# Performance work log

Hardware: AMD Instinct MI355X
Metric: run time of the kernel (lower is better)

The kernel has to match this reference:

```python
import jax, jax.numpy as jnp
import numpy as np

N = 50000      # nodes
E = 800000     # edges
F = 128        # input features
H = 128        # hidden dim
G = 1024       # graphs in batch
EPS = 1e-5


def setup_inputs() -> dict:
    key = jax.random.key(0)
    ks = jax.random.split(key, 16)
    s = 0.05
    return {
        "x": jax.random.normal(ks[0], (N, F), dtype=jnp.float32),
        "edge_index": jax.random.randint(ks[1], (2, E), 0, N, dtype=jnp.int64),
        "batch": jnp.sort(jax.random.randint(ks[2], (N,), 0, G, dtype=jnp.int64)),
        "convW0": jax.random.normal(ks[3], (F, H), dtype=jnp.float32) * s,
        "convW": jax.random.normal(ks[4], (2, H, H), dtype=jnp.float32) * s,  # layers 1,2
        "convb": jax.random.normal(ks[5], (3, H), dtype=jnp.float32) * s,
        "bn_gamma": jnp.ones((3, H), dtype=jnp.float32),
        "bn_beta": jnp.zeros((3, H), dtype=jnp.float32),
        "mW1": jax.random.normal(ks[6], (2 * H, 256), dtype=jnp.float32) * s,
        "mb1": jnp.zeros((256,), dtype=jnp.float32),
        "mW2": jax.random.normal(ks[7], (256, 128), dtype=jnp.float32) * s,
        "mb2": jnp.zeros((128,), dtype=jnp.float32),
        "mW3": jax.random.normal(ks[8], (128, 1), dtype=jnp.float32) * s,
        "mb3": jnp.zeros((1,), dtype=jnp.float32),
    }


def _gcn_norm(edge_index):
    # add self-loops, compute sym-normalization coeffs (PyG GCNConv default)
    loop = jnp.arange(N, dtype=edge_index.dtype)
    src = jnp.concatenate([edge_index[0], loop])
    dst = jnp.concatenate([edge_index[1], loop])
    deg = jax.ops.segment_sum(jnp.ones_like(dst, dtype=jnp.float32), dst, num_segments=N)
    dinv = jax.lax.rsqrt(deg)  # deg >= 1 due to self loops
    norm = dinv[src] * dinv[dst]  # [E+N]
    return src, dst, norm


def _gcn_layer(x, W, b, src, dst, norm):
    h = x @ W                               # [N, H]
    msg = h[src] * norm[:, None]            # gather + scale, [E+N, H]
    agg = jax.ops.segment_sum(msg, dst, num_segments=N)
    return agg + b


def _batchnorm(x, gamma, beta):
    mu = jnp.mean(x, axis=0)
    var = jnp.mean(jnp.square(x - mu), axis=0)  # biased, as torch training fwd
    return gamma * (x - mu) * jax.lax.rsqrt(var + EPS) + beta


def reference(x, edge_index, batch, convW0, convW, convb, bn_gamma, bn_beta,
              mW1, mb1, mW2, mb2, mW3, mb3):
    src, dst, norm = _gcn_norm(edge_index)
    Ws = [convW0, convW[0], convW[1]]
    for i in range(3):
        x = _gcn_layer(x, Ws[i], convb[i], src, dst, norm)
        x = _batchnorm(x, bn_gamma[i], bn_beta[i])
        x = jax.nn.relu(x)
        # dropout: identity in eval mode
    ones = jnp.ones((N,), dtype=x.dtype)
    counts = jax.ops.segment_sum(ones, batch, num_segments=G)  # [G]
    x_mean = jax.ops.segment_sum(x, batch, num_segments=G) / jnp.maximum(counts, 1.0)[:, None]
    x_max = jax.ops.segment_max(x, batch, num_segments=G)
    x_max = jnp.where(counts[:, None] > 0, x_max, 0.0)
    g = jnp.concatenate([x_mean, x_max], axis=1)  # [G, 2H]
    h = jax.nn.relu(g @ mW1 + mb1)
    h = jax.nn.relu(h @ mW2 + mb2)
    out = h @ mW3 + mb3                            # [G, 1]
    return out.squeeze(1)
```

## Files before the change

### kernel.cpp

```cpp
#include <hip/hip_runtime.h>


constexpr int FH = 128;
constexpr int GG = 1024;
constexpr int NAB = 2048;
constexpr int BKS = 1024;
constexpr int CPAD = 16;
constexpr int EPB = 4096;
constexpr float EPSV = 1e-5f;

typedef __attribute__((ext_vector_type(8))) short short8v;
typedef __attribute__((ext_vector_type(4))) float f32x4;

__device__ inline unsigned short bf16_rn(float x) {
    unsigned u = __float_as_uint(x);
    unsigned r = (u + 0x7FFFu + ((u >> 16) & 1u)) >> 16;
    return (unsigned short)r;
}
__device__ inline float bflo(unsigned u) { return __uint_as_float(u << 16); }
__device__ inline float bfhi(unsigned u) { return __uint_as_float(u & 0xFFFF0000u); }
__device__ inline float bfs(unsigned short h) { return __uint_as_float((unsigned)h << 16); }
__device__ inline float4 bf4tof(ushort4 h) {
    return make_float4(bfs(h.x), bfs(h.y), bfs(h.z), bfs(h.w));
}

__global__ void k_deg(const int* __restrict__ dst, unsigned* __restrict__ deg, int E) {
    int e = blockIdx.x * 256 + threadIdx.x;
    if (e < E) atomicAdd(&deg[dst[e]], 1u);
}

__global__ __launch_bounds__(1024) void k_scan1(const unsigned* __restrict__ deg,
                                                int* __restrict__ rowptr, int* __restrict__ bsum,
                                                float* __restrict__ dinv, int n) {
    __shared__ int wsum[16];
    int i = blockIdx.x * 1024 + threadIdx.x;
    int lane = threadIdx.x & 63, wid = threadIdx.x >> 6;
    int v = (i < n) ? (int)deg[i] : 0;
    if (i < n) dinv[i] = rsqrtf((float)v + 1.0f);
    int incl = v;
    #pragma unroll
    for (int off = 1; off < 64; off <<= 1) {
        int t = __shfl_up(incl, off, 64);
        if (lane >= off) incl += t;
    }
    if (lane == 63) wsum[wid] = incl;
    __syncthreads();
    int woff = 0;
    #pragma unroll
    for (int w = 0; w < 16; ++w) woff += (w < wid) ? wsum[w] : 0;
    if (i < n) rowptr[i] = woff + incl - v;
    if (threadIdx.x == 1023) bsum[blockIdx.x] = woff + incl;
}

__global__ void k_scan2(int* __restrict__ bsum, int* __restrict__ rowptr_n, int nb) {
    int lane = threadIdx.x;
    int v = (lane < nb) ? bsum[lane] : 0;
    int incl = v;
    #pragma unroll
    for (int off = 1; off < 64; off <<= 1) {
        int t = __shfl_up(incl, off, 64);
        if (lane >= off) incl += t;
    }
    if (lane < nb) bsum[lane] = incl - v;
    if (lane == 63) *rowptr_n = incl;
}

__global__ __launch_bounds__(1024) void k_scan3(int* __restrict__ rowptr,
                                                const int* __restrict__ bsum,
                                                int* __restrict__ bcur, int n) {
    int i = blockIdx.x * 1024 + threadIdx.x;
    if (i < n) {
        int r = rowptr[i] + bsum[blockIdx.x];
        rowptr[i] = r;
        if ((i & 63) == 0) bcur[(i >> 6) * CPAD] = r;
    }
}

__global__ __launch_bounds__(256) void k_binscatter(const int* __restrict__ src, const int* __restrict__ dst,
                                                    int* __restrict__ bcur, unsigned* __restrict__ tmp,
                                                    int E, int nbk) {
    __shared__ int hist[BKS];
    int tid = threadIdx.x;
    for (int b = tid; b < nbk; b += 256) hist[b] = 0;
    __syncthreads();
    int e0 = blockIdx.x * EPB;
    int s[16], d[16];
    #pragma unroll
    for (int i = 0; i < 16; ++i) {
        int e = e0 + i * 256 + tid;
        if (e < E) {
            s[i] = src[e]; d[i] = dst[e];
            atomicAdd(&hist[d[i] >> 6], 1);
        } else d[i] = -1;
    }
    __syncthreads();
    for (int b = tid; b < nbk; b += 256) {
        int c = hist[b];
        hist[b] = c ? atomicAdd(&bcur[b * CPAD], c) : 0;
    }
    __syncthreads();
    #pragma unroll
    for (int i = 0; i < 16; ++i) {
        if (d[i] >= 0) {
            int p = atomicAdd(&hist[d[i] >> 6], 1);
            tmp[p] = (unsigned)s[i] | ((unsigned)(d[i] & 63) << 16);
        }
    }
}

__global__ __launch_bounds__(256) void k_finesort(const unsigned* __restrict__ tmp,
                                                  const int* __restrict__ rowptr,
                                                  int* __restrict__ csr_src, int n) {
    __shared__ int cur[64];
    int nb0 = blockIdx.x << 6;
    int tid = threadIdx.x;
    int hi = min(nb0 + 64, n);
    if (tid < 64 && nb0 + tid < n) cur[tid] = rowptr[nb0 + tid];
    __syncthreads();
    int estart = rowptr[nb0], eend = rowptr[hi];
    for (int e = estart + tid; e < eend; e += 256) {
        unsigned pr = tmp[e];
        int p = atomicAdd(&cur[(pr >> 16) & 63], 1);
        csr_src[p] = (int)(pr & 0xFFFFu);
    }
}

__global__ void k_gptr(const int* __restrict__ batch, int* __restrict__ gptr, int n) {
    int g = blockIdx.x * 256 + threadIdx.x;
    if (g > GG) return;
    int lo = 0, hi = n;
    while (lo < hi) { int mid = (lo + hi) >> 1; if (batch[mid] < g) lo = mid + 1; else hi = mid; }
    gptr[g] = lo;
}

__global__ void k_wprep(const float* __restrict__ W0, const float* __restrict__ W12,
                        unsigned short* __restrict__ Wt) {
    int t = blockIdx.x * 256 + threadIdx.x;
    int l = t >> 14, o = t & 16383;
    const float* W = (l == 0) ? W0 : W12 + (size_t)(l - 1) * 16384;
    int j = o & 7, c = (o >> 3) & 15, hi = (o >> 7) & 3, kb = (o >> 9) & 3, nt = o >> 11;
    int k = kb * 32 + hi * 8 + j;
    int col = nt * 16 + c;
    Wt[t] = bf16_rn(W[k * 128 + col]);
}

template<bool BF16IN>
__global__ __launch_bounds__(256) void k_gemm(const void* __restrict__ Xp,
                                              const unsigned short* __restrict__ Wt,
                                              const float* __restrict__ dinv,
                                              const float* __restrict__ sc,
                                              const float* __restrict__ sh,
                                              unsigned short* __restrict__ H, int n) {
    int wave = threadIdx.x >> 6, L = threadIdx.x & 63;
    int hi = L >> 4, c16 = L & 15;
    int m0 = blockIdx.x * 64 + wave * 16;
    int arow = m0 + c16;
    bool okA = arow < n;

    short8v aF[4];
    #pragma unroll
    for (int kb = 0; kb < 4; ++kb) {
        int kc = kb * 32 + hi * 8;
        float v[8];
        #pragma unroll
        for (int j = 0; j < 8; ++j) v[j] = 0.f;
        if (okA) {
            if constexpr (BF16IN) {
                const unsigned short* Xb = (const unsigned short*)Xp;
                uint4 raw = *(const uint4*)&Xb[(size_t)arow * 128 + kc];
                v[0] = bflo(raw.x); v[1] = bfhi(raw.x);
                v[2] = bflo(raw.y); v[3] = bfhi(raw.y);
                v[4] = bflo(raw.z); v[5] = bfhi(raw.z);
                v[6] = bflo(raw.w); v[7] = bfhi(raw.w);
                float4 s0 = *(const float4*)&sc[kc], s1 = *(const float4*)&sc[kc + 4];
                float4 h0 = *(const float4*)&sh[kc], h1 = *(const float4*)&sh[kc + 4];
                v[0] = fmaxf(fmaf(v[0], s0.x, h0.x), 0.f);
                v[1] = fmaxf(fmaf(v[1], s0.y, h0.y), 0.f);
                v[2] = fmaxf(fmaf(v[2], s0.z, h0.z), 0.f);
                v[3] = fmaxf(fmaf(v[3], s0.w, h0.w), 0.f);
                v[4] = fmaxf(fmaf(v[4], s1.x, h1.x), 0.f);
                v[5] = fmaxf(fmaf(v[5], s1.y, h1.y), 0.f);
                v[6] = fmaxf(fmaf(v[6], s1.z, h1.z), 0.f);
                v[7] = fmaxf(fmaf(v[7], s1.w, h1.w), 0.f);
            } else {
                const float* Xf = (const float*)Xp;
                float4 v0 = *(const float4*)&Xf[(size_t)arow * 128 + kc];
                float4 v1 = *(const float4*)&Xf[(size_t)arow * 128 + kc + 4];
                v[0] = v0.x; v[1] = v0.y; v[2] = v0.z; v[3] = v0.w;
                v[4] = v1.x; v[5] = v1.y; v[6] = v1.z; v[7] = v1.w;
            }
        }
        short8v a;
        #pragma unroll
        for (int j = 0; j < 8; ++j) a[j] = (short)bf16_rn(v[j]);
        aF[kb] = a;
    }

    f32x4 acc[8];
    #pragma unroll
    for (int nt = 0; nt < 8; ++nt) {
        acc[nt][0] = 0.f; acc[nt][1] = 0.f; acc[nt][2] = 0.f; acc[nt][3] = 0.f;
    }
    #pragma unroll
    for (int nt = 0; nt < 8; ++nt) {
        #pragma unroll
        for (int kb = 0; kb < 4; ++kb) {
            short8v bF = *(const short8v*)&Wt[(size_t)(nt * 4 + kb) * 512 + L * 8];
            acc[nt] = __builtin_amdgcn_mfma_f32_16x16x32_bf16(aF[kb], bF, acc[nt], 0, 0, 0);
        }
    }

    #pragma unroll
    for (int reg = 0; reg < 4; ++reg) {
        int row = m0 + hi * 4 + reg;
        if (row < n) {
            float dv = dinv[row];
            #pragma unroll
            for (int nt = 0; nt < 8; ++nt)
                H[(size_t)row * 128 + nt * 16 + c16] = bf16_rn(acc[nt][reg] * dv);
        }
    }
}

__global__ __launch_bounds__(256) void k_aggstats(const int* __restrict__ rowptr, const int* __restrict__ csr_src,
                                                  const float* __restrict__ dinv,
                                                  const unsigned short* __restrict__ H2,
                                                  unsigned short* __restrict__ Bo,
                                                  float* __restrict__ partials, int n) {
    __shared__ float sb[8][128];
    int tid = threadIdx.x;
    int sub = tid >> 5, lane = tid & 31;
    const ushort4* Hv = (const ushort4*)H2;
    float sA[4] = {0.f, 0.f, 0.f, 0.f}, qA[4] = {0.f, 0.f, 0.f, 0.f};
    for (int node = blockIdx.x * 8 + sub; node < n; node += NAB * 8) {
        int beg = rowptr[node], end = rowptr[node + 1];
        float dv = dinv[node];
        float4 acc = bf4tof(Hv[(size_t)node * 32 + lane]);
        float4 acc2 = make_float4(0.f, 0.f, 0.f, 0.f);
        int e = beg;
        for (; e + 1 < end; e += 2) {
            int s0 = csr_src[e], s1 = csr_src[e + 1];
            float4 h0 = bf4tof(Hv[(size_t)s0 * 32 + lane]);
            float4 h1 = bf4tof(Hv[(size_t)s1 * 32 + lane]);
            acc.x += h0.x;  acc.y += h0.y;  acc.z += h0.z;  acc.w += h0.w;
            acc2.x += h1.x; acc2.y += h1.y; acc2.z += h1.z; acc2.w += h1.w;
        }
        if (e < end) {
            int s0 = csr_src[e];
            float4 h0 = bf4tof(Hv[(size_t)s0 * 32 + lane]);
            acc.x += h0.x; acc.y += h0.y; acc.z += h0.z; acc.w += h0.w;
        }
        ushort4 o;
        o.x = bf16_rn((acc.x + acc2.x) * dv);
        o.y = bf16_rn((acc.y + acc2.y) * dv);
        o.z = bf16_rn((acc.z + acc2.z) * dv);
        o.w = bf16_rn((acc.w + acc2.w) * dv);
        *(ushort4*)&Bo[(size_t)node * 128 + lane * 4] = o;
        float v0 = bfs(o.x), v1 = bfs(o.y), v2 = bfs(o.z), v3 = bfs(o.w);
        sA[0] += v0; qA[0] = fmaf(v0, v0, qA[0]);
        sA[1] += v1; qA[1] = fmaf(v1, v1, qA[1]);
        sA[2] += v2; qA[2] = fmaf(v2, v2, qA[2]);
        sA[3] += v3; qA[3] = fmaf(v3, v3, qA[3]);
    }
    #pragma unroll
    for (int j = 0; j < 4; ++j) sb[sub][lane * 4 + j] = sA[j];
    __syncthreads();
    if (tid < 128) partials[(size_t)blockIdx.x * 256 + tid] =
        sb[0][tid] + sb[1][tid] + sb[2][tid] + sb[3][tid] +
        sb[4][tid] + sb[5][tid] + sb[6][tid] + sb[7][tid];
    __syncthreads();
    #pragma unroll
    for (int j = 0; j < 4; ++j) sb[sub][lane * 4 + j] = qA[j];
    __syncthreads();
    if (tid < 128) partials[(size_t)blockIdx.x * 256 + 128 + tid] =
        sb[0][tid] + sb[1][tid] + sb[2][tid] + sb[3][tid] +
        sb[4][tid] + sb[5][tid] + sb[6][tid] + sb[7][tid];
}

__global__ __launch_bounds__(256) void k_finstats(const float* __restrict__ partials,
                                                  const float* __restrict__ gamma, const float* __restrict__ beta,
                                                  float* __restrict__ sc, float* __restrict__ sh, int n) {
    __shared__ float red[256];
    int f = blockIdx.x;
    int t = threadIdx.x;
    int half = t >> 7, idx = t & 127;
    float acc = 0.f;
    for (int b = idx; b < NAB; b += 128)
        acc += partials[(size_t)b * 256 + half * 128 + f];
    red[t] = acc;
    __syncthreads();
    #pragma unroll
    for (int off = 64; off; off >>= 1) {
        if (idx < off) red[t] += red[t + off];
        __syncthreads();
    }
    if (t == 0) {
        float s = red[0], q = red[128];
        float invN = 1.0f / (float)n;
        float mu = s * invN;
        float var = fmaf(-mu, mu, q * invN);
        float scale = gamma[f] * rsqrtf(var + EPSV);
        sc[f] = scale;
        sh[f] = fmaf(-mu, scale, beta[f]);
    }
}

__global__ __launch_bounds__(256) void k_pool(const unsigned short* __restrict__ X, const int* __restrict__ gptr,
                                              const float* __restrict__ sc, const float* __restrict__ sh,
                                              float* __restrict__ pooled) {
    __shared__ float shm[256];
    int g = blockIdx.x;
    int t = threadIdx.x;
    int f = t & 127, sub = t >> 7;
    int beg = gptr[g], end = gptr[g + 1];
    float scf = sc[f], shf = sh[f];
    float s = 0.f, m = 0.f;
    for (int r = beg + sub; r < end; r += 2) {
        float xv = bfs(X[(size_t)r * 128 + f]);
        float v = fmaxf(fmaf(xv, scf, shf), 0.f);
        s += v; m = fmaxf(m, v);
    }
    shm[t] = s;
    __syncthreads();
    if (sub == 0) {
        int c = end - beg;
        float inv = (c > 0) ? 1.0f / (float)c : 0.f;
        pooled[(size_t)g * 256 + f] = (s + shm[t + 128]) * inv;
    }
    __syncthreads();
    shm[t] = m;
    __syncthreads();
    if (sub == 1) {
        pooled[(size_t)g * 256 + 128 + f] = fmaxf(m, shm[t - 128]);
    }
}

__global__ __launch_bounds__(256) void k_mlp1(const float* __restrict__ pooled, const float* __restrict__ W1,
                                              const float* __restrict__ b1, float* __restrict__ H1) {
    __shared__ float grow[256];
    int gi = blockIdx.x, t = threadIdx.x;
    grow[t] = pooled[(size_t)gi * 256 + t];
    __syncthreads();
    float acc = b1[t];
    #pragma unroll 8
    for (int k = 0; k < 256; ++k) acc = fmaf(grow[k], W1[k * 256 + t], acc);
    H1[gi * 256 + t] = fmaxf(acc, 0.f);
}

__global__ __launch_bounds__(128) void k_mlp23(const float* __restrict__ H1, const float* __restrict__ W2,
                                               const float* __restrict__ b2, const float* __restrict__ W3,
                                               const float* __restrict__ b3, float* __restrict__ out) {
    __shared__ float row[256];
    __shared__ float wred[2];
    int gi = blockIdx.x, t = threadIdx.x;
    row[t] = H1[gi * 256 + t];
    row[t + 128] = H1[gi * 256 + t + 128];
    __syncthreads();
    float acc = b2[t];
    #pragma unroll 8
    for (int k = 0; k < 256; ++k) acc = fmaf(row[k], W2[k * 128 + t], acc);
    float v = fmaxf(acc, 0.f) * W3[t];
    #pragma unroll
    for (int off = 32; off; off >>= 1) v += __shfl_down(v, off);
    if ((t & 63) == 0) wred[t >> 6] = v;
    __syncthreads();
    if (t == 0) out[gi] = wred[0] + wred[1] + b3[0];
}

extern "C" void kernel_launch(void* const* d_in, const int* in_sizes, int n_in,
                              void* d_out, int out_size, void* d_ws, size_t ws_size,
                              hipStream_t stream) {
    const float* x      = (const float*)d_in[0];
    const int*   ei     = (const int*)d_in[1];
    const int*   batch  = (const int*)d_in[2];
    const float* convW0 = (const float*)d_in[3];
    const float* convW  = (const float*)d_in[4];
    const float* gamma  = (const float*)d_in[6];
    const float* beta   = (const float*)d_in[7];
    const float* mW1    = (const float*)d_in[8];
    const float* mb1    = (const float*)d_in[9];
    const float* mW2    = (const float*)d_in[10];
    const float* mb2    = (const float*)d_in[11];
    const float* mW3    = (const float*)d_in[12];
    const float* mb3    = (const float*)d_in[13];
    float* out = (float*)d_out;

    const int E = in_sizes[1] / 2;
    const int n = in_sizes[0] / FH;
    const int npad = (n + 4) & ~3;
    const int nb = (n + 1023) / 1024;
    const int nbk = (n + 63) >> 6;

    float*          A     = (float*)d_ws;
    unsigned short* H2b   = (unsigned short*)A;
    unsigned*       tmp   = (unsigned*)A;
    float*    B       = A + (size_t)n * FH;
    unsigned short* Bb = (unsigned short*)B;
    int*      bcur    = (int*)B;
    float*    dinv    = B + (size_t)n * FH;
    unsigned* deg     = (unsigned*)(dinv + n);
    float*    parts   = (float*)(deg + n);
    float*    sc      = parts + (size_t)NAB * 256;
    float*    sh      = sc + 128;
    float*    pooled  = sh + 128;
    float*    h1      = pooled + (size_t)GG * 256;
    int*      gptr    = (int*)(h1 + (size_t)GG * 256);
    int*      rowptr  = gptr + ((GG + 4) & ~3);
    int*      bsum    = rowptr + npad;
    int*      csrsrc  = bsum + 64;
    unsigned short* Wt = (unsigned short*)(csrsrc + ((E + 3) & ~3));

    const int* srcI = ei;
    const int* dstI = ei + E;

    hipMemsetAsync(deg, 0, (size_t)n * sizeof(unsigned), stream);
    k_deg<<<(E + 255) / 256, 256, 0, stream>>>(dstI, deg, E);
    k_scan1<<<nb, 1024, 0, stream>>>(deg, rowptr, bsum, dinv, n);
    k_scan2<<<1, 64, 0, stream>>>(bsum, rowptr + n, nb);
    k_scan3<<<nb, 1024, 0, stream>>>(rowptr, bsum, bcur, n);
    k_binscatter<<<(E + EPB - 1) / EPB, 256, 0, stream>>>(srcI, dstI, bcur, tmp, E, nbk);
    k_finesort<<<nbk, 256, 0, stream>>>(tmp, rowptr, csrsrc, n);
    k_gptr<<<(GG + 1 + 255) / 256, 256, 0, stream>>>(batch, gptr, n);
    k_wprep<<<3 * 16384 / 256, 256, 0, stream>>>(convW0, convW, Wt);

    for (int l = 0; l < 3; ++l) {
        if (l == 0)
            k_gemm<false><<<(n + 63) / 64, 256, 0, stream>>>(x, Wt, dinv, nullptr, nullptr, H2b, n);
        else
            k_gemm<true><<<(n + 63) / 64, 256, 0, stream>>>(Bb, Wt + (size_t)l * 16384, dinv, sc, sh, H2b, n);
        k_aggstats<<<NAB, 256, 0, stream>>>(rowptr, csrsrc, dinv, H2b, Bb, parts, n);
        k_finstats<<<FH, 256, 0, stream>>>(parts, gamma + l * FH, beta + l * FH, sc, sh, n);
    }

    k_pool<<<GG, 256, 0, stream>>>(Bb, gptr, sc, sh, pooled);
    k_mlp1<<<GG, 256, 0, stream>>>(pooled, mW1, mb1, h1);
    k_mlp23<<<GG, 128, 0, stream>>>(h1, mW2, mb2, mW3, mb3, out);
}
```

Before: 390.4 us.

## Fuse setup kernels, fold scan2 into scan3, and merge pooling with MLP head

Measured after the change: 371.2 us. 4.9% less time.

```diff
diff --git a/kernel.cpp b/kernel.cpp
--- a/kernel.cpp
+++ b/kernel.cpp
@@ -24,9 +24,27 @@
     return make_float4(bfs(h.x), bfs(h.y), bfs(h.z), bfs(h.w));
 }
 
-__global__ void k_deg(const int* __restrict__ dst, unsigned* __restrict__ deg, int E) {
-    int e = blockIdx.x * 256 + threadIdx.x;
-    if (e < E) atomicAdd(&deg[dst[e]], 1u);
+__global__ __launch_bounds__(256) void k_setup(const int* __restrict__ dst, unsigned* __restrict__ deg, int E,
+                                               const int* __restrict__ batch, int* __restrict__ gptr, int n,
+                                               const float* __restrict__ W0, const float* __restrict__ W12,
+                                               unsigned short* __restrict__ Wt, int degB, int gptrB) {
+    int b = blockIdx.x;
+    if (b < degB) {
+        int e = b * 256 + threadIdx.x;
+        if (e < E) atomicAdd(&deg[dst[e]], 1u);
+    } else if (b < degB + gptrB) {
+        int g = (b - degB) * 256 + threadIdx.x;
+        if (g > GG) return;
+        int lo = 0, hi = n;
+        while (lo < hi) { int mid = (lo + hi) >> 1; if (batch[mid] < g) lo = mid + 1; else hi = mid; }
+        gptr[g] = lo;
+    } else {
+        int t = (b - degB - gptrB) * 256 + threadIdx.x;
+        int l = t >> 14, o = t & 16383;
+        const float* W = (l == 0) ? W0 : W12 + (size_t)(l - 1) * 16384;
+        int j = o & 7, c = (o >> 3) & 15, hi = (o >> 7) & 3, kb = (o >> 9) & 3, nt = o >> 11;
+        Wt[t] = bf16_rn(W[(kb * 32 + hi * 8 + j) * 128 + nt * 16 + c]);
+    }
 }
 
 __global__ __launch_bounds__(1024) void k_scan1(const unsigned* __restrict__ deg,
@@ -52,27 +70,23 @@
     if (threadIdx.x == 1023) bsum[blockIdx.x] = woff + incl;
 }
 
-__global__ void k_scan2(int* __restrict__ bsum, int* __restrict__ rowptr_n, int nb) {
-    int lane = threadIdx.x;
-    int v = (lane < nb) ? bsum[lane] : 0;
-    int incl = v;
-    #pragma unroll
-    for (int off = 1; off < 64; off <<= 1) {
-        int t = __shfl_up(incl, off, 64);
-        if (lane >= off) incl += t;
-    }
-    if (lane < nb) bsum[lane] = incl - v;
-    if (lane == 63) *rowptr_n = incl;
-}
-
 __global__ __launch_bounds__(1024) void k_scan3(int* __restrict__ rowptr,
                                                 const int* __restrict__ bsum,
+                                                const unsigned* __restrict__ deg,
                                                 int* __restrict__ bcur, int n) {
+    __shared__ int s_off;
+    if (threadIdx.x == 0) {
+        int off = 0;
+        for (int w = 0; w < (int)blockIdx.x; ++w) off += bsum[w];
+        s_off = off;
+    }
+    __syncthreads();
     int i = blockIdx.x * 1024 + threadIdx.x;
     if (i < n) {
-        int r = rowptr[i] + bsum[blockIdx.x];
+        int r = rowptr[i] + s_off;
         rowptr[i] = r;
         if ((i & 63) == 0) bcur[(i >> 6) * CPAD] = r;
+        if (i == n - 1) rowptr[n] = r + (int)deg[i];
     }
 }
 
@@ -123,25 +137,6 @@
         int p = atomicAdd(&cur[(pr >> 16) & 63], 1);
         csr_src[p] = (int)(pr & 0xFFFFu);
     }
-}
-
-__global__ void k_gptr(const int* __restrict__ batch, int* __restrict__ gptr, int n) {
-    int g = blockIdx.x * 256 + threadIdx.x;
-    if (g > GG) return;
-    int lo = 0, hi = n;
-    while (lo < hi) { int mid = (lo + hi) >> 1; if (batch[mid] < g) lo = mid + 1; else hi = mid; }
-    gptr[g] = lo;
-}
-
-__global__ void k_wprep(const float* __restrict__ W0, const float* __restrict__ W12,
-                        unsigned short* __restrict__ Wt) {
-    int t = blockIdx.x * 256 + threadIdx.x;
-    int l = t >> 14, o = t & 16383;
-    const float* W = (l == 0) ? W0 : W12 + (size_t)(l - 1) * 16384;
-    int j = o & 7, c = (o >> 3) & 15, hi = (o >> 7) & 3, kb = (o >> 9) & 3, nt = o >> 11;
-    int k = kb * 32 + hi * 8 + j;
-    int col = nt * 16 + c;
-    Wt[t] = bf16_rn(W[k * 128 + col]);
 }
 
 template<bool BF16IN>
@@ -305,19 +300,23 @@
     }
 }
 
-__global__ __launch_bounds__(256) void k_pool(const unsigned short* __restrict__ X, const int* __restrict__ gptr,
+__global__ __launch_bounds__(256) void k_tail(const unsigned short* __restrict__ X, const int* __restrict__ gptr,
                                               const float* __restrict__ sc, const float* __restrict__ sh,
-                                              float* __restrict__ pooled) {
+                                              const float* __restrict__ W1, const float* __restrict__ b1,
+                                              const float* __restrict__ W2, const float* __restrict__ b2,
+                                              const float* __restrict__ W3, const float* __restrict__ b3,
+                                              float* __restrict__ out) {
+    __shared__ float grow[256];
     __shared__ float shm[256];
-    int g = blockIdx.x;
-    int t = threadIdx.x;
+    __shared__ float h1s[256];
+    __shared__ float wred[2];
+    int g = blockIdx.x, t = threadIdx.x;
     int f = t & 127, sub = t >> 7;
     int beg = gptr[g], end = gptr[g + 1];
     float scf = sc[f], shf = sh[f];
     float s = 0.f, m = 0.f;
     for (int r = beg + sub; r < end; r += 2) {
-        float xv = bfs(X[(size_t)r * 128 + f]);
-        float v = fmaxf(fmaf(xv, scf, shf), 0.f);
+        float v = fmaxf(fmaf(bfs(X[(size_t)r * 128 + f]), scf, shf), 0.f);
         s += v; m = fmaxf(m, v);
     }
     shm[t] = s;
@@ -325,46 +324,29 @@
     if (sub == 0) {
         int c = end - beg;
         float inv = (c > 0) ? 1.0f / (float)c : 0.f;
-        pooled[(size_t)g * 256 + f] = (s + shm[t + 128]) * inv;
+        grow[f] = (s + shm[t + 128]) * inv;
     }
     __syncthreads();
     shm[t] = m;
     __syncthreads();
-    if (sub == 1) {
-        pooled[(size_t)g * 256 + 128 + f] = fmaxf(m, shm[t - 128]);
-    }
-}
-
-__global__ __launch_bounds__(256) void k_mlp1(const float* __restrict__ pooled, const float* __restrict__ W1,
-                                              const float* __restrict__ b1, float* __restrict__ H1) {
-    __shared__ float grow[256];
-    int gi = blockIdx.x, t = threadIdx.x;
-    grow[t] = pooled[(size_t)gi * 256 + t];
-    __syncthreads();
-    float acc = b1[t];
+    if (sub == 1) grow[128 + f] = fmaxf(m, shm[t - 128]);
+    __syncthreads();
+    float a1 = b1[t];
     #pragma unroll 8
-    for (int k = 0; k < 256; ++k) acc = fmaf(grow[k], W1[k * 256 + t], acc);
-    H1[gi * 256 + t] = fmaxf(acc, 0.f);
-}
-
-__global__ __launch_bounds__(128) void k_mlp23(const float* __restrict__ H1, const float* __restrict__ W2,
-                                               const float* __restrict__ b2, const float* __restrict__ W3,
-                                               const float* __restrict__ b3, float* __restrict__ out) {
-    __shared__ float row[256];
-    __shared__ float wred[2];
-    int gi = blockIdx.x, t = threadIdx.x;
-    row[t] = H1[gi * 256 + t];
-    row[t + 128] = H1[gi * 256 + t + 128];
-    __syncthreads();
-    float acc = b2[t];
-    #pragma unroll 8
-    for (int k = 0; k < 256; ++k) acc = fmaf(row[k], W2[k * 128 + t], acc);
-    float v = fmaxf(acc, 0.f) * W3[t];
-    #pragma unroll
-    for (int off = 32; off; off >>= 1) v += __shfl_down(v, off);
-    if ((t & 63) == 0) wred[t >> 6] = v;
-    __syncthreads();
-    if (t == 0) out[gi] = wred[0] + wred[1] + b3[0];
+    for (int k = 0; k < 256; ++k) a1 = fmaf(grow[k], W1[k * 256 + t], a1);
+    h1s[t] = fmaxf(a1, 0.f);
+    __syncthreads();
+    if (t < 128) {
+        float a2 = b2[t];
+        #pragma unroll 8
+        for (int k = 0; k < 256; ++k) a2 = fmaf(h1s[k], W2[k * 128 + t], a2);
+        float v = fmaxf(a2, 0.f) * W3[t];
+        #pragma unroll
+        for (int off = 32; off; off >>= 1) v += __shfl_down(v, off);
+        if ((t & 63) == 0) wred[t >> 6] = v;
+    }
+    __syncthreads();
+    if (t == 0) out[g] = wred[0] + wred[1] + b3[0];
 }
 
 extern "C" void kernel_launch(void* const* d_in, const int* in_sizes, int n_in,
@@ -402,9 +384,7 @@
     float*    parts   = (float*)(deg + n);
     float*    sc      = parts + (size_t)NAB * 256;
     float*    sh      = sc + 128;
-    float*    pooled  = sh + 128;
-    float*    h1      = pooled + (size_t)GG * 256;
-    int*      gptr    = (int*)(h1 + (size_t)GG * 256);
+    int*      gptr    = (int*)(sh + 128);
     int*      rowptr  = gptr + ((GG + 4) & ~3);
     int*      bsum    = rowptr + npad;
     int*      csrsrc  = bsum + 64;
@@ -413,15 +393,17 @@
     const int* srcI = ei;
     const int* dstI = ei + E;
 
+    const int degB  = (E + 255) / 256;
+    const int gptrB = (GG + 1 + 255) / 256;
+    const int wprepB = 3 * 16384 / 256;
+
     hipMemsetAsync(deg, 0, (size_t)n * sizeof(unsigned), stream);
-    k_deg<<<(E + 255) / 256, 256, 0, stream>>>(dstI, deg, E);
+    k_setup<<<degB + gptrB + wprepB, 256, 0, stream>>>(dstI, deg, E, batch, gptr, n,
+                                                       convW0, convW, Wt, degB, gptrB);
     k_scan1<<<nb, 1024, 0, stream>>>(deg, rowptr, bsum, dinv, n);
-    k_scan2<<<1, 64, 0, stream>>>(bsum, rowptr + n, nb);
-    k_scan3<<<nb, 1024, 0, stream>>>(rowptr, bsum, bcur, n);
+    k_scan3<<<nb, 1024, 0, stream>>>(rowptr, bsum, deg, bcur, n);
     k_binscatter<<<(E + EPB - 1) / EPB, 256, 0, stream>>>(srcI, dstI, bcur, tmp, E, nbk);
     k_finesort<<<nbk, 256, 0, stream>>>(tmp, rowptr, csrsrc, n);
-    k_gptr<<<(GG + 1 + 255) / 256, 256, 0, stream>>>(batch, gptr, n);
-    k_wprep<<<3 * 16384 / 256, 256, 0, stream>>>(convW0, convW, Wt);
 
     for (int l = 0; l < 3; ++l) {
         if (l == 0)
@@ -432,7 +414,5 @@
         k_finstats<<<FH, 256, 0, stream>>>(parts, gamma + l * FH, beta + l * FH, sc, sh, n);
     }
 
-    k_pool<<<GG, 256, 0, stream>>>(Bb, gptr, sc, sh, pooled);
-    k_mlp1<<<GG, 256, 0, stream>>>(pooled, mW1, mb1, h1);
-    k_mlp23<<<GG, 128, 0, stream>>>(h1, mW2, mb2, mW3, mb3, out);
-}
+    k_tail<<<GG, 256, 0, stream>>>(Bb, gptr, sc, sh, mW1, mb1, mW2, mb2, mW3, mb3, out);
+}
```
